# Kernel tuning notes

Hardware: AMD Instinct MI355X
Metric: run time of the kernel (lower is better)

## Reference

```python
import jax, jax.numpy as jnp
import numpy as np

B, N_TOKENS, D, K = 16, 4096, 256, 4096
COMMITMENT_COST = 0.25


def setup_inputs() -> dict:
    key = jax.random.key(0)
    k1, k2 = jax.random.split(key)
    x = jax.random.normal(k1, (B, N_TOKENS, D), dtype=jnp.float32)
    # nn.Embedding init uniform(-1/K, 1/K); scale is irrelevant to correctness,
    # use the same distribution for fidelity.
    codebook = jax.random.uniform(k2, (K, D), dtype=jnp.float32,
                                  minval=-1.0 / K, maxval=1.0 / K)
    return {"x": x, "codebook": codebook}


def reference(x, codebook):
    Bb, Nn, Dd = x.shape
    x_flat = x.reshape(-1, Dd)                                    # [BN, D]
    dist_sq = (jnp.sum(x_flat * x_flat, axis=1, keepdims=True)
               + jnp.sum(codebook * codebook, axis=1)
               - 2.0 * x_flat @ codebook.T)                       # [BN, K]
    dist_sq = jnp.maximum(dist_sq, 0.0)
    idx = jnp.argmin(dist_sq, axis=1)                             # [BN]
    q_flat = codebook[idx]                                        # [BN, D]
    q = q_flat.reshape(x.shape)

    x_sg = jax.lax.stop_gradient(x_flat)
    q_sg = jax.lax.stop_gradient(q_flat)
    codebook_loss = jnp.mean((q_flat - x_sg) ** 2, axis=-1).reshape(Bb, Nn)
    commit_loss = jnp.mean((x_flat - q_sg) ** 2, axis=-1).reshape(Bb, Nn)
    per_token_loss = codebook_loss + COMMITMENT_COST * commit_loss
    mean_vq_loss = jnp.mean(per_token_loss)

    q_st = x + jax.lax.stop_gradient(q - x)                       # straight-through

    counts = jnp.zeros((codebook.shape[0],), dtype=jnp.float32).at[idx].add(1.0)
    avg_probs = counts / x_flat.shape[0]
    perplexity = jnp.exp(-jnp.sum(avg_probs * jnp.log(avg_probs + 1e-10)))

    return q_st, mean_vq_loss, perplexity, idx
```

## Files before the change

kernel.cpp:

```cpp
#include <hip/hip_runtime.h>
#include <hip/hip_bf16.h>
#include <cstdint>
#include <cstddef>

#define D 256
#define NTOK 65536
#define KCODES 4096
#define Q_ELEMS (NTOK * D)
#define DELTA 3.0e-4f
#define CAP 24

typedef short bf16x8 __attribute__((ext_vector_type(8)));
typedef float f32x4 __attribute__((ext_vector_type(4)));
typedef unsigned short ushort8 __attribute__((ext_vector_type(8)));

__device__ __forceinline__ void gload_lds16(const float* g, float* l) {
  __builtin_amdgcn_global_load_lds(
      (const __attribute__((address_space(1))) void*)(g),
      (__attribute__((address_space(3))) void*)(l), 16, 0, 0);
}
__device__ __forceinline__ unsigned short f2bf(float f) {
  __hip_bfloat16 h = __float2bfloat16(f);
  unsigned short u;
  __builtin_memcpy(&u, &h, 2);
  return u;
}
__device__ __forceinline__ float bf2f(unsigned short u) {
  __hip_bfloat16 h;
  __builtin_memcpy(&h, &u, 2);
  return __bfloat162float(h);
}

__global__ __launch_bounds__(256) void ee_kernel(const float* __restrict__ cb,
                                                 float* __restrict__ se) {
  const int row = blockIdx.x * 4 + (threadIdx.x >> 6);
  const int lane = threadIdx.x & 63;
  const float4 v = reinterpret_cast<const float4*>(cb + (size_t)row * D)[lane];
  double s = (double)v.x * v.x + (double)v.y * v.y +
             (double)v.z * v.z + (double)v.w * v.w;
#pragma unroll
  for (int o = 32; o > 0; o >>= 1) s += __shfl_down(s, o, 64);
  if (lane == 0) se[row] = (float)s;
}

__global__ __launch_bounds__(256) void xx_kernel(const float* __restrict__ x,
                                                 float* __restrict__ sx) {
  const int row = blockIdx.x * 4 + (threadIdx.x >> 6);
  const int lane = threadIdx.x & 63;
  const float4 v = reinterpret_cast<const float4*>(x + (size_t)row * D)[lane];
  double s = (double)v.x * v.x + (double)v.y * v.y +
             (double)v.z * v.z + (double)v.w * v.w;
#pragma unroll
  for (int o = 32; o > 0; o >>= 1) s += __shfl_down(s, o, 64);
  if (lane == 0) sx[row] = (float)s;
}

__global__ __launch_bounds__(256) void pack_e_kernel(const float* __restrict__ cb,
                                                     unsigned short* __restrict__ bpack) {
  const int gid = blockIdx.x * 256 + threadIdx.x;
  const int c = gid >> 2;
  const int kt = gid & 3;
  const int row = c & 127;
  const int swz = (row & 7) << 3;
  unsigned short* dst = bpack + ((size_t)((c >> 7) * 4 + kt)) * 8192 + row * 64;
  const float* src = cb + (size_t)c * D + kt * 64;
#pragma unroll
  for (int j = 0; j < 8; ++j) {
    ushort8 o;
#pragma unroll
    for (int e = 0; e < 8; ++e) o[e] = f2bf(src[j * 8 + e]);
    *reinterpret_cast<ushort8*>(dst + ((j * 8) ^ swz)) = o;
  }
}

__global__ __launch_bounds__(256, 2) void screen5_kernel(
    const float* __restrict__ x, const unsigned short* __restrict__ bpack,
    const float* __restrict__ se, unsigned int* __restrict__ ccnt_g,
    unsigned int* __restrict__ cand_g, float* __restrict__ rm_g) {
  __shared__ __attribute__((aligned(16))) unsigned short bbuf[3][8192];
  __shared__ __attribute__((aligned(16))) unsigned short se_lds[KCODES];
  __shared__ unsigned int cand[128][CAP];
  __shared__ unsigned int ccnt[128];

  const int tid = threadIdx.x;
  const int lane = tid & 63;
  const int w = tid >> 6;
  const int l15 = lane & 15;
  const int kg = lane >> 4;
  const int tok0 = blockIdx.x * 128;

  if (tid < 128) ccnt[tid] = 0;
  {
    const float4* s4 = reinterpret_cast<const float4*>(se) + tid * 4;
    const float4 a = s4[0], b = s4[1], c = s4[2], d = s4[3];
    ushort8 o0, o1;
    o0[0] = f2bf(a.x); o0[1] = f2bf(a.y); o0[2] = f2bf(a.z); o0[3] = f2bf(a.w);
    o0[4] = f2bf(b.x); o0[5] = f2bf(b.y); o0[6] = f2bf(b.z); o0[7] = f2bf(b.w);
    o1[0] = f2bf(c.x); o1[1] = f2bf(c.y); o1[2] = f2bf(c.z); o1[3] = f2bf(c.w);
    o1[4] = f2bf(d.x); o1[5] = f2bf(d.y); o1[6] = f2bf(d.z); o1[7] = f2bf(d.w);
    *reinterpret_cast<ushort8*>(&se_lds[tid * 16]) = o0;
    *reinterpret_cast<ushort8*>(&se_lds[tid * 16 + 8]) = o1;
  }

  bf16x8 ah[2][8];
#pragma unroll
  for (int gi = 0; gi < 2; ++gi) {
    const int t = tok0 + w * 32 + gi * 16 + l15;
    const float* xp = x + (size_t)t * D;
#pragma unroll
    for (int ks = 0; ks < 8; ++ks) {
      const float4 v0 = *reinterpret_cast<const float4*>(xp + ks * 32 + kg * 8);
      const float4 v1 = *reinterpret_cast<const float4*>(xp + ks * 32 + kg * 8 + 4);
      const float xv[8] = {v0.x, v0.y, v0.z, v0.w, v1.x, v1.y, v1.z, v1.w};
      bf16x8 h;
#pragma unroll
      for (int e = 0; e < 8; ++e) h[e] = (short)f2bf(xv[e]);
      ah[gi][ks] = h;
    }
  }

  auto STAGE = [&](int u) {
    const char* s = (const char*)bpack + (size_t)u * 16384 + w * 4096 + lane * 16;
    char* d = (char*)&bbuf[u % 3][0] + w * 4096;
    gload_lds16((const float*)s, (float*)d);
    gload_lds16((const float*)(s + 1024), (float*)(d + 1024));
    gload_lds16((const float*)(s + 2048), (float*)(d + 2048));
    gload_lds16((const float*)(s + 3072), (float*)(d + 3072));
  };

  float rm[2][4];
#pragma unroll
  for (int fr = 0; fr < 2; ++fr)
#pragma unroll
    for (int q = 0; q < 4; ++q) rm[fr][q] = 3.4e38f;

  f32x4 acc[2][8];

  __builtin_amdgcn_sched_barrier(0);
  asm volatile("s_waitcnt vmcnt(0)" ::: "memory");
  STAGE(0);
  STAGE(1);
  asm volatile("s_waitcnt vmcnt(4) lgkmcnt(0)" ::: "memory");
  __builtin_amdgcn_s_barrier();
  __builtin_amdgcn_sched_barrier(0);

  for (int ct4 = 0; ct4 < 32; ++ct4) {
#pragma unroll
    for (int kt = 0; kt < 4; ++kt) {
      const int u = ct4 * 4 + kt;
      if (u + 2 < 128) STAGE(u + 2);
      if (kt == 0) {
#pragma unroll
        for (int fr = 0; fr < 2; ++fr)
#pragma unroll
          for (int fc = 0; fc < 8; ++fc) acc[fr][fc] = (f32x4){0.f, 0.f, 0.f, 0.f};
      }
      const unsigned short* bb = &bbuf[u % 3][0];
#pragma unroll
      for (int kh = 0; kh < 2; ++kh) {
        const int ks = kt * 2 + kh;
        bf16x8 bfrag[8];
#pragma unroll
        for (int fc = 0; fc < 8; ++fc) {
          const int row = fc * 16 + l15;
          const int off = row * 64 + ((kh * 32 + kg * 8) ^ ((row & 7) << 3));
          bfrag[fc] = *reinterpret_cast<const bf16x8*>(bb + off);
        }
#pragma unroll
        for (int fr = 0; fr < 2; ++fr)
#pragma unroll
          for (int fc = 0; fc < 8; ++fc)
            acc[fr][fc] = __builtin_amdgcn_mfma_f32_16x16x32_bf16(
                ah[fr][ks], bfrag[fc], acc[fr][fc], 0, 0, 0);
      }
      if (kt == 3) {
        float sef[8];
#pragma unroll
        for (int fc = 0; fc < 8; ++fc)
          sef[fc] = bf2f(se_lds[ct4 * 128 + fc * 16 + l15]);
#pragma unroll
        for (int fr = 0; fr < 2; ++fr)
#pragma unroll
          for (int q = 0; q < 4; ++q) {
            float m = fmaf(-2.0f, acc[fr][0][q], sef[0]);
#pragma unroll
            for (int fc = 1; fc < 8; ++fc)
              m = fminf(m, fmaf(-2.0f, acc[fr][fc][q], sef[fc]));
            m = fminf(m, __shfl_xor(m, 1, 64));
            m = fminf(m, __shfl_xor(m, 2, 64));
            m = fminf(m, __shfl_xor(m, 4, 64));
            m = fminf(m, __shfl_xor(m, 8, 64));
            rm[fr][q] = fminf(rm[fr][q], m);
            const float thr = rm[fr][q] + DELTA;
            const int tl = w * 32 + fr * 16 + kg * 4 + q;
#pragma unroll
            for (int fc = 0; fc < 8; ++fc) {
              const float s = fmaf(-2.0f, acc[fr][fc][q], sef[fc]);
              if (s <= thr) {
                const unsigned p = atomicAdd(&ccnt[tl], 1u);
                if (p < CAP)
                  cand[tl][p] = ((unsigned)f2bf(s) << 16) |
                                (unsigned)(ct4 * 128 + fc * 16 + l15);
              }
            }
          }
      }
      if (u != 127) {
        if (u != 126) asm volatile("s_waitcnt vmcnt(4)" ::: "memory");
        else          asm volatile("s_waitcnt vmcnt(0)" ::: "memory");
        __builtin_amdgcn_s_barrier();
        __builtin_amdgcn_sched_barrier(0);
      }
    }
  }

  __syncthreads();
  if (tid < 128) ccnt_g[tok0 + tid] = ccnt[tid];
  if (l15 == 0) {
#pragma unroll
    for (int fr = 0; fr < 2; ++fr)
#pragma unroll
      for (int q = 0; q < 4; ++q)
        rm_g[tok0 + w * 32 + fr * 16 + kg * 4 + q] = rm[fr][q];
  }
  for (int j = tid; j < 128 * CAP; j += 256)
    cand_g[(size_t)tok0 * CAP + j] = cand[j / CAP][j % CAP];
}

__global__ __launch_bounds__(256) void rescore_kernel(
    const float* __restrict__ x, const float* __restrict__ cb,
    const float* __restrict__ se, const unsigned int* __restrict__ ccnt_g,
    const unsigned int* __restrict__ cand_g, const float* __restrict__ rm_g,
    int* __restrict__ idx_i, float* __restrict__ idxf_out,
    unsigned int* __restrict__ ovf_count, int* __restrict__ ovf_list) {
  const int t = blockIdx.x * 256 + threadIdx.x;
  const unsigned n = ccnt_g[t];
  if (n > CAP) {
    const unsigned p = atomicAdd(ovf_count, 1u);
    ovf_list[p] = t;
    return;
  }
  const float4* xp = reinterpret_cast<const float4*>(x + (size_t)t * D);
  double sxd = 0.0;
  for (int d4 = 0; d4 < 64; ++d4) {
    const float4 v = xp[d4];
    sxd += (double)v.x * v.x + (double)v.y * v.y +
           (double)v.z * v.z + (double)v.w * v.w;
  }
  const float sxv = (float)sxd;
  const float thr = rm_g[t] + DELTA;
  float bq = 3.4e38f;
  int bc = 0x7fffffff;
  for (unsigned k = 0; k < n; ++k) {
    const unsigned pk = cand_g[(size_t)t * CAP + k];
    if (bf2f((unsigned short)(pk >> 16)) > thr) continue;
    const int c = (int)(pk & 0xFFFFu);
    const float4* cp = reinterpret_cast<const float4*>(cb + (size_t)c * D);
    float acc = 0.0f;
#pragma unroll 8
    for (int d4 = 0; d4 < 64; ++d4) {
      const float4 xv = xp[d4];
      const float4 ev = cp[d4];
      acc = fmaf(xv.x, ev.x, acc);
      acc = fmaf(xv.y, ev.y, acc);
      acc = fmaf(xv.z, ev.z, acc);
      acc = fmaf(xv.w, ev.w, acc);
    }
    const float r = sxv + se[c];
    const float q = r - 2.0f * acc;
    if (q < bq || (q == bq && c < bc)) { bq = q; bc = c; }
  }
  idx_i[t] = bc;
  idxf_out[t] = (float)bc;
}

__global__ __launch_bounds__(256) void ovf_kernel(
    const float* __restrict__ x, const float* __restrict__ cb,
    const float* __restrict__ se, const unsigned int* __restrict__ ovf_count,
    const int* __restrict__ ovf_list, int* __restrict__ idx_i,
    float* __restrict__ idxf_out) {
  __shared__ float bvv[256];
  __shared__ int bii[256];
  __shared__ double shd[256];
  const int tid = threadIdx.x;
  const unsigned cnt = *ovf_count;
  for (unsigned i = blockIdx.x; i < cnt; i += gridDim.x) {
    const int t = ovf_list[i];
    const float xv1 = x[(size_t)t * D + tid];
    shd[tid] = (double)xv1 * xv1;
    __syncthreads();
    for (int o = 128; o > 0; o >>= 1) {
      if (tid < o) shd[tid] += shd[tid + o];
      __syncthreads();
    }
    const float sxv = (float)shd[0];
    __syncthreads();
    const float4* xp = reinterpret_cast<const float4*>(x + (size_t)t * D);
    float bq = 3.4e38f;
    int bc = 0x7fffffff;
    for (int c = tid; c < KCODES; c += 256) {
      const float4* cp = reinterpret_cast<const float4*>(cb + (size_t)c * D);
      float acc = 0.0f;
#pragma unroll 8
      for (int d4 = 0; d4 < 64; ++d4) {
        const float4 xv = xp[d4];
        const float4 ev = cp[d4];
        acc = fmaf(xv.x, ev.x, acc);
        acc = fmaf(xv.y, ev.y, acc);
        acc = fmaf(xv.z, ev.z, acc);
        acc = fmaf(xv.w, ev.w, acc);
      }
      const float r = sxv + se[c];
      const float q = r - 2.0f * acc;
      if (q < bq || (q == bq && c < bc)) { bq = q; bc = c; }
    }
    bvv[tid] = bq;
    bii[tid] = bc;
    __syncthreads();
    for (int o = 128; o > 0; o >>= 1) {
      if (tid < o) {
        const float v2 = bvv[tid + o];
        const int c2 = bii[tid + o];
        if (v2 < bvv[tid] || (v2 == bvv[tid] && c2 < bii[tid])) {
          bvv[tid] = v2;
          bii[tid] = c2;
        }
      }
      __syncthreads();
    }
    if (tid == 0) {
      idx_i[t] = bii[0];
      idxf_out[t] = (float)bii[0];
    }
    __syncthreads();
  }
}

__global__ __launch_bounds__(256) void argmin_fb_kernel(const float* __restrict__ x,
                                                        const float* __restrict__ cb,
                                                        const float* __restrict__ se,
                                                        const float* __restrict__ sx,
                                                        int* __restrict__ idx_out,
                                                        float* __restrict__ idxf_out) {
  __shared__ __attribute__((aligned(16))) float xs[64 * 128];
  __shared__ __attribute__((aligned(16))) float es[64 * 128];
  const int tid = threadIdx.x;
  const int lane = tid & 63;
  const int w = tid >> 6;
  const int wt = w & 1;
  const int wc = w >> 1;
  const int tgl = lane & 7;
  const int cgl = lane >> 3;
  const int t0 = wt * 64 + tgl * 8;
  const int c0 = wc * 64 + cgl * 8;
  const int tok0 = blockIdx.x * 128;
  float sxf[8];
#pragma unroll
  for (int i = 0; i < 8; ++i) sxf[i] = sx[tok0 + t0 + i];
  float bv[8];
  int bi[8];
#pragma unroll
  for (int i = 0; i < 8; ++i) { bv[i] = 3.4e38f; bi[i] = 0; }
  for (int ct = 0; ct < KCODES / 128; ++ct) {
    float acc[8][8] = {};
    for (int kt = 0; kt < 4; ++kt) {
      __syncthreads();
      {
        const float* xsrc = x + (size_t)tok0 * D + kt * 64;
        const float* esrc = cb + (size_t)(ct * 128) * D + kt * 64;
#pragma unroll
        for (int p = 0; p < 8; ++p) {
          const int idx = p * 256 + tid;
          const int t = idx >> 4;
          const int c = idx & 15;
          const int colp = (t + 8 * (c >> 1)) & 127;
          const float4 xv = *reinterpret_cast<const float4*>(xsrc + (size_t)t * D + c * 4);
          float* xd = &xs[(c * 4) * 128 + colp];
          xd[0] = xv.x; xd[128] = xv.y; xd[256] = xv.z; xd[384] = xv.w;
          const float4 ev = *reinterpret_cast<const float4*>(esrc + (size_t)t * D + c * 4);
          float* ed = &es[(c * 4) * 128 + colp];
          ed[0] = ev.x; ed[128] = ev.y; ed[256] = ev.z; ed[384] = ev.w;
        }
      }
      __syncthreads();
      for (int kp = 0; kp < 8; ++kp) {
        const float* xb = &xs[(kp * 8) * 128 + ((t0 + 8 * kp) & 127)];
        const float* eb = &es[(kp * 8) * 128 + ((c0 + 8 * kp) & 127)];
#pragma unroll
        for (int k2 = 0; k2 < 8; ++k2) {
          const float4 xv0 = *reinterpret_cast<const float4*>(xb + k2 * 128);
          const float4 xv1 = *reinterpret_cast<const float4*>(xb + k2 * 128 + 4);
          const float4 ev0 = *reinterpret_cast<const float4*>(eb + k2 * 128);
          const float4 ev1 = *reinterpret_cast<const float4*>(eb + k2 * 128 + 4);
          const float xa[8] = {xv0.x, xv0.y, xv0.z, xv0.w, xv1.x, xv1.y, xv1.z, xv1.w};
          const float ea[8] = {ev0.x, ev0.y, ev0.z, ev0.w, ev1.x, ev1.y, ev1.z, ev1.w};
#pragma unroll
          for (int i = 0; i < 8; ++i)
#pragma unroll
            for (int j = 0; j < 8; ++j) acc[i][j] = fmaf(xa[i], ea[j], acc[i][j]);
        }
      }
    }
#pragma unroll
    for (int j = 0; j < 8; ++j) {
      const int cidx = ct * 128 + c0 + j;
      const float sef = se[cidx];
#pragma unroll
      for (int i = 0; i < 8; ++i) {
        const float r = sxf[i] + sef;
        const float s = r - 2.0f * acc[i][j];
        if (s < bv[i]) { bv[i] = s; bi[i] = cidx; }
      }
    }
  }
  __syncthreads();
  float* red_val = xs;
  int* red_idx = reinterpret_cast<int*>(xs + 128 * 17);
  const int g = wc * 8 + cgl;
#pragma unroll
  for (int i = 0; i < 8; ++i) {
    red_val[(t0 + i) * 17 + g] = bv[i];
    red_idx[(t0 + i) * 17 + g] = bi[i];
  }
  __syncthreads();
  if (tid < 128) {
    float v = red_val[tid * 17 + 0];
    int ix = red_idx[tid * 17 + 0];
#pragma unroll
    for (int gg = 1; gg < 16; ++gg) {
      const float vv = red_val[tid * 17 + gg];
      const int ii = red_idx[tid * 17 + gg];
      if (vv < v || (vv == v && ii < ix)) { v = vv; ix = ii; }
    }
    idx_out[tok0 + tid] = ix;
    idxf_out[tok0 + tid] = (float)ix;
  }
}

__global__ __launch_bounds__(256) void finalize_kernel(const float* __restrict__ x,
                                                       const float* __restrict__ cb,
                                                       const int* __restrict__ idx,
                                                       float* __restrict__ q_out,
                                                       unsigned int* __restrict__ counts,
                                                       double* __restrict__ partials) {
  __shared__ double tok_s[16];
  const int tid = threadIdx.x;
  const int lt = tid >> 4;
  const int ld = tid & 15;
  const int t = blockIdx.x * 16 + lt;
  const int id = idx[t];
  const float* xp = x + (size_t)t * D + ld * 16;
  const float* ep = cb + (size_t)id * D + ld * 16;
  float* qp = q_out + (size_t)t * D + ld * 16;
  float s = 0.0f;
#pragma unroll
  for (int c = 0; c < 4; ++c) {
    const float4 xv = reinterpret_cast<const float4*>(xp)[c];
    const float4 ev = reinterpret_cast<const float4*>(ep)[c];
    const float d0 = ev.x - xv.x, d1 = ev.y - xv.y;
    const float d2 = ev.z - xv.z, d3 = ev.w - xv.w;
    s = fmaf(d0, d0, s);
    s = fmaf(d1, d1, s);
    s = fmaf(d2, d2, s);
    s = fmaf(d3, d3, s);
    float4 qv;
    qv.x = xv.x + d0;
    qv.y = xv.y + d1;
    qv.z = xv.z + d2;
    qv.w = xv.w + d3;
    reinterpret_cast<float4*>(qp)[c] = qv;
  }
#pragma unroll
  for (int o = 8; o > 0; o >>= 1) s += __shfl_down(s, o, 16);
  if (ld == 0) {
    atomicAdd(&counts[id], 1u);
    tok_s[lt] = (double)s;
  }
  __syncthreads();
  if (tid == 0) {
    double bs = 0.0;
    for (int i = 0; i < 16; ++i) bs += tok_s[i];
    partials[blockIdx.x] = bs;
  }
}

__global__ __launch_bounds__(256) void final_kernel(const unsigned int* __restrict__ counts,
                                                    const double* __restrict__ partials,
                                                    float* __restrict__ loss_out,
                                                    float* __restrict__ perp_out) {
  __shared__ double sh[256];
  const int tid = threadIdx.x;
  double ls = 0.0;
  for (int i = tid; i < NTOK / 16; i += 256) ls += partials[i];
  sh[tid] = ls;
  __syncthreads();
#pragma unroll
  for (int o = 128; o > 0; o >>= 1) {
    if (tid < o) sh[tid] += sh[tid + o];
    __syncthreads();
  }
  if (tid == 0) *loss_out = (float)(sh[0] * (1.25 / (256.0 * 65536.0)));
  __syncthreads();
  double hs = 0.0;
  for (int i = tid; i < KCODES; i += 256) {
    const float p = (float)counts[i] / 65536.0f;
    hs += (double)(p * logf(p + 1e-10f));
  }
  sh[tid] = hs;
  __syncthreads();
#pragma unroll
  for (int o = 128; o > 0; o >>= 1) {
    if (tid < o) sh[tid] += sh[tid + o];
    __syncthreads();
  }
  if (tid == 0) *perp_out = expf((float)(-sh[0]));
}

extern "C" void kernel_launch(void* const* d_in, const int* in_sizes, int n_in,
                              void* d_out, int out_size, void* d_ws, size_t ws_size,
                              hipStream_t stream) {
  (void)in_sizes; (void)n_in; (void)out_size;
  const float* x = (const float*)d_in[0];
  const float* cb = (const float*)d_in[1];

  float* out = (float*)d_out;
  float* q_out = out;
  float* loss_out = out + (size_t)Q_ELEMS;
  float* perp_out = out + (size_t)Q_ELEMS + 1;
  float* idxf_out = out + (size_t)Q_ELEMS + 2;

  char* ws = (char*)d_ws;
  float* se = (float*)(ws + 0);
  unsigned int* counts = (unsigned int*)(ws + (16 << 10));
  double* partials = (double*)(ws + (32 << 10));
  int* idx_i = (int*)(ws + (128 << 10));
  float* sx = (float*)(ws + (384 << 10));
  unsigned int* ovf_count = (unsigned int*)(ws + (640 << 10));
  int* ovf_list = (int*)(ws + (644 << 10));
  unsigned int* ccnt_g = (unsigned int*)(ws + (1 << 20));
  float* rm_g = (float*)(ws + (3 << 19));
  unsigned int* cand_g = (unsigned int*)(ws + (2 << 20));
  unsigned short* bpack = (unsigned short*)(ws + (12 << 20));

  hipMemsetAsync(counts, 0, KCODES * sizeof(unsigned int), stream);
  hipMemsetAsync(ovf_count, 0, sizeof(unsigned int), stream);
  ee_kernel<<<KCODES / 4, 256, 0, stream>>>(cb, se);

  if (ws_size >= (size_t)20 * 1024 * 1024) {
    pack_e_kernel<<<64, 256, 0, stream>>>(cb, bpack);
    screen5_kernel<<<NTOK / 128, 256, 0, stream>>>(x, bpack, se, ccnt_g, cand_g,
                                                   rm_g);
    rescore_kernel<<<NTOK / 256, 256, 0, stream>>>(x, cb, se, ccnt_g, cand_g,
                                                   rm_g, idx_i, idxf_out,
                                                   ovf_count, ovf_list);
    ovf_kernel<<<64, 256, 0, stream>>>(x, cb, se, ovf_count, ovf_list,
                                       idx_i, idxf_out);
  } else {
    xx_kernel<<<NTOK / 4, 256, 0, stream>>>(x, sx);
    argmin_fb_kernel<<<NTOK / 128, 256, 0, stream>>>(x, cb, se, sx, idx_i, idxf_out);
  }
  finalize_kernel<<<NTOK / 16, 256, 0, stream>>>(x, cb, idx_i, q_out, counts, partials);
  final_kernel<<<1, 256, 0, stream>>>(counts, partials, loss_out, perp_out);
}
```

Measured before the change: 358.1 us.

## Skip rescoring for single-survivor tokens and simplify screen kernel barriers

The rescore kernel first counts candidates under the threshold and, when exactly one survives, takes it directly without computing the token norm or any exact dot products. The screen kernel's hand-tuned partial vmcnt waits and raw s_barrier calls are replaced by plain __syncthreads after each stage. The first part avoids reading x and codebook rows for most tokens. The second may serialize the three-buffer prefetch pipeline, because __syncthreads waits for all outstanding loads.

Measured after the change: 345.9 us. 3.4% less time.

```diff
diff --git a/kernel.cpp b/kernel.cpp
--- a/kernel.cpp
+++ b/kernel.cpp
@@ -73,7 +73,7 @@
   }
 }
 
-__global__ __launch_bounds__(256, 2) void screen5_kernel(
+__global__ __launch_bounds__(256, 2) void screen3_kernel(
     const float* __restrict__ x, const unsigned short* __restrict__ bpack,
     const float* __restrict__ se, unsigned int* __restrict__ ccnt_g,
     unsigned int* __restrict__ cand_g, float* __restrict__ rm_g) {
@@ -136,13 +136,9 @@
 
   f32x4 acc[2][8];
 
-  __builtin_amdgcn_sched_barrier(0);
-  asm volatile("s_waitcnt vmcnt(0)" ::: "memory");
   STAGE(0);
   STAGE(1);
-  asm volatile("s_waitcnt vmcnt(4) lgkmcnt(0)" ::: "memory");
-  __builtin_amdgcn_s_barrier();
-  __builtin_amdgcn_sched_barrier(0);
+  __syncthreads();
 
   for (int ct4 = 0; ct4 < 32; ++ct4) {
 #pragma unroll
@@ -205,16 +201,10 @@
             }
           }
       }
-      if (u != 127) {
-        if (u != 126) asm volatile("s_waitcnt vmcnt(4)" ::: "memory");
-        else          asm volatile("s_waitcnt vmcnt(0)" ::: "memory");
-        __builtin_amdgcn_s_barrier();
-        __builtin_amdgcn_sched_barrier(0);
-      }
-    }
-  }
-
-  __syncthreads();
+      __syncthreads();
+    }
+  }
+
   if (tid < 128) ccnt_g[tok0 + tid] = ccnt[tid];
   if (l15 == 0) {
 #pragma unroll
@@ -240,35 +230,49 @@
     ovf_list[p] = t;
     return;
   }
-  const float4* xp = reinterpret_cast<const float4*>(x + (size_t)t * D);
-  double sxd = 0.0;
-  for (int d4 = 0; d4 < 64; ++d4) {
-    const float4 v = xp[d4];
-    sxd += (double)v.x * v.x + (double)v.y * v.y +
-           (double)v.z * v.z + (double)v.w * v.w;
-  }
-  const float sxv = (float)sxd;
   const float thr = rm_g[t] + DELTA;
-  float bq = 3.4e38f;
-  int bc = 0x7fffffff;
+  int surv = 0;
+  int only_c = 0x7fffffff;
   for (unsigned k = 0; k < n; ++k) {
     const unsigned pk = cand_g[(size_t)t * CAP + k];
-    if (bf2f((unsigned short)(pk >> 16)) > thr) continue;
-    const int c = (int)(pk & 0xFFFFu);
-    const float4* cp = reinterpret_cast<const float4*>(cb + (size_t)c * D);
-    float acc = 0.0f;
+    if (bf2f((unsigned short)(pk >> 16)) <= thr) {
+      ++surv;
+      only_c = (int)(pk & 0xFFFFu);
+    }
+  }
+  int bc;
+  if (surv == 1) {
+    bc = only_c;
+  } else {
+    const float4* xp = reinterpret_cast<const float4*>(x + (size_t)t * D);
+    double sxd = 0.0;
+    for (int d4 = 0; d4 < 64; ++d4) {
+      const float4 v = xp[d4];
+      sxd += (double)v.x * v.x + (double)v.y * v.y +
+             (double)v.z * v.z + (double)v.w * v.w;
+    }
+    const float sxv = (float)sxd;
+    float bq = 3.4e38f;
+    bc = 0x7fffffff;
+    for (unsigned k = 0; k < n; ++k) {
+      const unsigned pk = cand_g[(size_t)t * CAP + k];
+      if (bf2f((unsigned short)(pk >> 16)) > thr) continue;
+      const int c = (int)(pk & 0xFFFFu);
+      const float4* cp = reinterpret_cast<const float4*>(cb + (size_t)c * D);
+      float acc = 0.0f;
 #pragma unroll 8
-    for (int d4 = 0; d4 < 64; ++d4) {
-      const float4 xv = xp[d4];
-      const float4 ev = cp[d4];
-      acc = fmaf(xv.x, ev.x, acc);
-      acc = fmaf(xv.y, ev.y, acc);
-      acc = fmaf(xv.z, ev.z, acc);
-      acc = fmaf(xv.w, ev.w, acc);
-    }
-    const float r = sxv + se[c];
-    const float q = r - 2.0f * acc;
-    if (q < bq || (q == bq && c < bc)) { bq = q; bc = c; }
+      for (int d4 = 0; d4 < 64; ++d4) {
+        const float4 xv = xp[d4];
+        const float4 ev = cp[d4];
+        acc = fmaf(xv.x, ev.x, acc);
+        acc = fmaf(xv.y, ev.y, acc);
+        acc = fmaf(xv.z, ev.z, acc);
+        acc = fmaf(xv.w, ev.w, acc);
+      }
+      const float r = sxv + se[c];
+      const float q = r - 2.0f * acc;
+      if (q < bq || (q == bq && c < bc)) { bq = q; bc = c; }
+    }
   }
   idx_i[t] = bc;
   idxf_out[t] = (float)bc;
@@ -548,7 +552,7 @@
 
   if (ws_size >= (size_t)20 * 1024 * 1024) {
     pack_e_kernel<<<64, 256, 0, stream>>>(cb, bpack);
-    screen5_kernel<<<NTOK / 128, 256, 0, stream>>>(x, bpack, se, ccnt_g, cand_g,
+    screen3_kernel<<<NTOK / 128, 256, 0, stream>>>(x, bpack, se, ccnt_g, cand_g,
                                                    rm_g);
     rescore_kernel<<<NTOK / 256, 256, 0, stream>>>(x, cb, se, ccnt_g, cand_g,
                                                    rm_g, idx_i, idxf_out,
```
